# Kernel optimization log

Measured on AMD Instinct MI355X. Metric: run time of the kernel, lower is better.

The kernel has to match this reference:

```python
import jax, jax.numpy as jnp
import numpy as np

IN_SIZE, OUT_SIZE, EDGE_SIZE = 32, 32, 16
NET_LAYERS = [128, 128]          # cfg.net_layers (hidden sizes of the edge MLP)
B, N_NEIGH = 10000, 20           # nodes x neighbors
E = B * N_NEIGH                  # total edges


def setup_inputs() -> dict:
    key = jax.random.key(0)
    ks = jax.random.split(key, 16)
    h_v = jax.random.normal(ks[0], (B, N_NEIGH), jnp.float32)
    h_w = jax.random.normal(ks[1], (B, IN_SIZE), jnp.float32)
    e_vw = jax.random.normal(ks[2], (E, EDGE_SIZE), jnp.float32)
    dims = [EDGE_SIZE] + NET_LAYERS + [IN_SIZE * OUT_SIZE]
    params = {}
    for i, (din, dout) in enumerate(zip(dims[:-1], dims[1:])):
        bound = 1.0 / np.sqrt(din)  # torch nn.Linear default init
        params[f"W{i}"] = jax.random.uniform(ks[3 + 2 * i], (dout, din), jnp.float32, -bound, bound)
        params[f"b{i}"] = jax.random.uniform(ks[4 + 2 * i], (dout,), jnp.float32, -bound, bound)
    return {"h_v": h_v, "h_w": h_w, "e_vw": e_vw, **params}


def reference(h_v, h_w, e_vw, W0, b0, W1, b1, W2, b2):
    # Edge MLP: edge_size -> 128 -> 128 -> in*out (ReLU on hidden layers only)
    x = jax.nn.relu(e_vw @ W0.T + b0)
    x = jax.nn.relu(x @ W1.T + b1)
    m = (x @ W2.T + b2).reshape(-1, OUT_SIZE, IN_SIZE)  # [E, out, in]

    # Faithful reproduction of h_w[..., None].expand(B, in, n).view(-1, in)
    n = h_v.shape[1]
    h_w_rows = jnp.broadcast_to(h_w[:, :, None], (h_w.shape[0], IN_SIZE, n)).reshape(-1, IN_SIZE)  # [E, in]

    # bmm(m, h_w_rows[..., None]).squeeze() -> [E, out]
    out = jnp.einsum("eoi,ei->eo", m, h_w_rows)
    return jnp.squeeze(out)
```

## Files before the change

kernel.cpp:

```cpp
#include <hip/hip_runtime.h>


typedef __bf16 bf16x8 __attribute__((ext_vector_type(8)));
typedef float  f32x4  __attribute__((ext_vector_type(4)));

#define NB       10000
#define NNEIGH   20
#define PADH     136
#define NCHUNK   25

#define WS_W0S   0
#define WS_W1B   8192
#define WS_W2G   40960
#define WS_B2G   532480

__device__ __forceinline__ unsigned short f2bf(float f) {
    unsigned int u = __float_as_uint(f);
    unsigned int r = (u + 0x7fffu + ((u >> 16) & 1u)) >> 16;
    return (unsigned short)r;
}
__device__ __forceinline__ unsigned int pack2(float a, float b) {
    return (unsigned int)f2bf(a) | ((unsigned int)f2bf(b) << 16);
}

__global__ __launch_bounds__(256) void prep_kernel(
    const float* __restrict__ W0, const float* __restrict__ W1,
    const float* __restrict__ W2, const float* __restrict__ b2,
    unsigned short* __restrict__ w0s, unsigned short* __restrict__ w1b,
    unsigned short* __restrict__ w2g, float* __restrict__ b2g)
{
    const int bx = blockIdx.x, tid = threadIdx.x;
    if (bx < 960) {
        int gid = bx * 256 + tid;
        int kn = gid / 12288, rem = gid % 12288;
        int c = rem >> 7, k = rem & 127;
        int g = c >> 5, o = c & 31;
        int j0 = (32 * kn) / 20;
        int lo = 20 * (j0 + g) - 32 * kn;     if (lo < 0) lo = 0;
        int hi = 20 * (j0 + g + 1) - 32 * kn; if (hi > 32) hi = 32;
        float s = 0.f;
        for (int i = lo; i < hi; ++i) s += W2[(size_t)(32 * o + i) * 128 + k];
        w2g[gid] = f2bf(s);
    } else if (bx == 960) {
        for (int idx = tid; idx < 1920; idx += 256) {
            int kn = idx / 96, rem = idx - kn * 96;
            int g = rem >> 5, o = rem & 31;
            int j0 = (32 * kn) / 20;
            int lo = 20 * (j0 + g) - 32 * kn;     if (lo < 0) lo = 0;
            int hi = 20 * (j0 + g + 1) - 32 * kn; if (hi > 32) hi = 32;
            float s = 0.f;
            for (int i = lo; i < hi; ++i) s += b2[32 * o + i];
            b2g[idx] = s;
        }
    } else if (bx <= 962) {
        for (int i2 = tid; i2 < 2048; i2 += 256) {
            int idx = (bx - 961) * 2048 + i2;
            int ct = idx >> 9, lane = (idx >> 3) & 63, j = idx & 7;
            int lq = lane & 15, q = lane >> 4;
            int k = q * 8 + j;
            w0s[idx] = (k < 16) ? f2bf(W0[(ct * 16 + lq) * 16 + k]) : (unsigned short)0;
        }
    } else {
        int base = (bx - 963) * 1024;
        for (int i2 = tid; i2 < 1024; i2 += 256)
            w1b[base + i2] = f2bf(W1[base + i2]);
    }
}

__global__ __launch_bounds__(256, 2) void msg_kernel(
    const float* __restrict__ h_w, const float* __restrict__ e_vw,
    const float* __restrict__ b0v, const float* __restrict__ b1v,
    const unsigned short* __restrict__ w0s, const unsigned short* __restrict__ w1b,
    const unsigned short* __restrict__ w2g, const float* __restrict__ b2g,
    float* __restrict__ out)
{
    __shared__ __align__(16) unsigned short sW1[128 * PADH];
    __shared__ __align__(16) unsigned short sW2g[96 * PADH];
    __shared__ __align__(16) unsigned short sX[64 * PADH];

    const int tid = threadIdx.x;
    const int lane = tid & 63, w = tid >> 6;
    const int quad = lane >> 4, lq = lane & 15;
    const int kn = blockIdx.y, chunk = blockIdx.x;
    const int j0 = (32 * kn) / 20;

    {
        const uint4* src = (const uint4*)w1b;
        uint4* dst = (uint4*)sW1;
        for (int i = tid; i < 2048; i += 256) { int r = i >> 4, c = i & 15; dst[r * 17 + c] = src[i]; }
    }
    {
        const uint4* src = (const uint4*)(w2g + (size_t)kn * 96 * 128);
        uint4* dst = (uint4*)sW2g;
        for (int i = tid; i < 1536; i += 256) { int r = i >> 4, c = i & 15; dst[r * 17 + c] = src[i]; }
    }

    bf16x8 w0f[8];
#pragma unroll
    for (int ct = 0; ct < 8; ++ct)
        w0f[ct] = *(const bf16x8*)(w0s + (ct * 64 + lane) * 8);
    float b0r[8], b1r[8];
#pragma unroll
    for (int ct = 0; ct < 8; ++ct) {
        b0r[ct] = b0v[ct * 16 + lq];
        b1r[ct] = b1v[ct * 16 + lq];
    }
    float b2r[6];
#pragma unroll
    for (int i = 0; i < 6; ++i) {
        int g = i >> 1, half = i & 1;
        b2r[i] = b2g[kn * 96 + g * 32 + half * 16 + lq];
    }
    __syncthreads();

    const int rbase = w * 16;

    for (int btile = chunk; btile < 157; btile += NCHUNK) {
        const int bbase = btile * 64;
        const int rowE = bbase + rbase + lq;

        union { bf16x8 v; uint4 u; } A;
        A.u = make_uint4(0u, 0u, 0u, 0u);
        if (quad < 2 && rowE < NB) {
            const float4* p = (const float4*)(e_vw + ((size_t)rowE * NNEIGH + kn) * 16 + quad * 8);
            float4 f0 = p[0], f1 = p[1];
            A.u = make_uint4(pack2(f0.x, f0.y), pack2(f0.z, f0.w),
                             pack2(f1.x, f1.y), pack2(f1.z, f1.w));
        }

        float hwv[4][3];
#pragma unroll
        for (int r2 = 0; r2 < 4; ++r2) {
            int b = bbase + rbase + quad * 4 + r2;
#pragma unroll
            for (int g = 0; g < 3; ++g) {
                int jv = j0 + g; if (jv > 31) jv = 31;
                hwv[r2][g] = (b < NB) ? h_w[b * 32 + jv] : 0.f;
            }
        }

#pragma unroll
        for (int ct = 0; ct < 8; ++ct) {
            f32x4 acc = {0.f, 0.f, 0.f, 0.f};
            acc = __builtin_amdgcn_mfma_f32_16x16x32_bf16(A.v, w0f[ct], acc, 0, 0, 0);
#pragma unroll
            for (int r2 = 0; r2 < 4; ++r2) {
                float v = acc[r2] + b0r[ct];
                v = v > 0.f ? v : 0.f;
                sX[(rbase + quad * 4 + r2) * PADH + ct * 16 + lq] = f2bf(v);
            }
        }

        {
            bf16x8 af[4];
#pragma unroll
            for (int ka = 0; ka < 4; ++ka)
                af[ka] = *(const bf16x8*)&sX[(rbase + lq) * PADH + ka * 32 + quad * 8];
#pragma unroll
            for (int ct = 0; ct < 8; ++ct) {
                f32x4 acc = {0.f, 0.f, 0.f, 0.f};
#pragma unroll
                for (int ka = 0; ka < 4; ++ka) {
                    bf16x8 bf = *(const bf16x8*)&sW1[(ct * 16 + lq) * PADH + ka * 32 + quad * 8];
                    acc = __builtin_amdgcn_mfma_f32_16x16x32_bf16(af[ka], bf, acc, 0, 0, 0);
                }
#pragma unroll
                for (int r2 = 0; r2 < 4; ++r2) {
                    float v = acc[r2] + b1r[ct];
                    v = v > 0.f ? v : 0.f;
                    sX[(rbase + quad * 4 + r2) * PADH + ct * 16 + lq] = f2bf(v);
                }
            }
        }

        {
            bf16x8 af[4];
#pragma unroll
            for (int ka = 0; ka < 4; ++ka)
                af[ka] = *(const bf16x8*)&sX[(rbase + lq) * PADH + ka * 32 + quad * 8];
            f32x4 accC[6];
#pragma unroll
            for (int ct = 0; ct < 6; ++ct) {
                f32x4 acc = {0.f, 0.f, 0.f, 0.f};
#pragma unroll
                for (int ka = 0; ka < 4; ++ka) {
                    bf16x8 bf = *(const bf16x8*)&sW2g[(ct * 16 + lq) * PADH + ka * 32 + quad * 8];
                    acc = __builtin_amdgcn_mfma_f32_16x16x32_bf16(af[ka], bf, acc, 0, 0, 0);
                }
                accC[ct] = acc;
            }
#pragma unroll
            for (int half = 0; half < 2; ++half) {
#pragma unroll
                for (int r2 = 0; r2 < 4; ++r2) {
                    int b = bbase + rbase + quad * 4 + r2;
                    float oval = 0.f;
#pragma unroll
                    for (int g = 0; g < 3; ++g)
                        oval += hwv[r2][g] * (accC[g * 2 + half][r2] + b2r[g * 2 + half]);
                    if (b < NB)
                        out[((size_t)b * NNEIGH + kn) * 32 + half * 16 + lq] = oval;
                }
            }
        }
    }
}

extern "C" void kernel_launch(void* const* d_in, const int* in_sizes, int n_in,
                              void* d_out, int out_size, void* d_ws, size_t ws_size,
                              hipStream_t stream)
{
    const float* h_w = (const float*)d_in[1];
    const float* e_vw = (const float*)d_in[2];
    const float* W0 = (const float*)d_in[3];
    const float* b0 = (const float*)d_in[4];
    const float* W1 = (const float*)d_in[5];
    const float* b1 = (const float*)d_in[6];
    const float* W2 = (const float*)d_in[7];
    const float* b2 = (const float*)d_in[8];
    float* out = (float*)d_out;

    char* ws = (char*)d_ws;
    unsigned short* w0s = (unsigned short*)(ws + WS_W0S);
    unsigned short* w1b = (unsigned short*)(ws + WS_W1B);
    unsigned short* w2g = (unsigned short*)(ws + WS_W2G);
    float*          b2g = (float*)(ws + WS_B2G);

    prep_kernel<<<979, 256, 0, stream>>>(W0, W1, W2, b2, w0s, w1b, w2g, b2g);
    dim3 grid(NCHUNK, 20);
    msg_kernel<<<grid, 256, 0, stream>>>(h_w, e_vw, b0, b1, w0s, w1b, w2g, b2g, out);
}
```

Measured before the change: 134.2 us.

## Transpose MFMA operands, fold biases into accumulators, keep W2 in registers

New measurement: 183.7 us. +36.9%, slower.

```diff
diff --git a/kernel.cpp b/kernel.cpp
--- a/kernel.cpp
+++ b/kernel.cpp
@@ -6,7 +6,7 @@
 
 #define NB       10000
 #define NNEIGH   20
-#define PADH     136
+#define PADH     132
 #define NCHUNK   25
 
 #define WS_W0S   0
@@ -24,24 +24,48 @@
 }
 
 __global__ __launch_bounds__(256) void prep_kernel(
-    const float* __restrict__ W0, const float* __restrict__ W1,
+    const float* __restrict__ W0, const float* __restrict__ b0,
+    const float* __restrict__ W1,
     const float* __restrict__ W2, const float* __restrict__ b2,
     unsigned short* __restrict__ w0s, unsigned short* __restrict__ w1b,
     unsigned short* __restrict__ w2g, float* __restrict__ b2g)
 {
     const int bx = blockIdx.x, tid = threadIdx.x;
-    if (bx < 960) {
+    if (bx < 16) {
         int gid = bx * 256 + tid;
-        int kn = gid / 12288, rem = gid % 12288;
-        int c = rem >> 7, k = rem & 127;
-        int g = c >> 5, o = c & 31;
-        int j0 = (32 * kn) / 20;
-        int lo = 20 * (j0 + g) - 32 * kn;     if (lo < 0) lo = 0;
-        int hi = 20 * (j0 + g + 1) - 32 * kn; if (hi > 32) hi = 32;
-        float s = 0.f;
-        for (int i = lo; i < hi; ++i) s += W2[(size_t)(32 * o + i) * 128 + k];
-        w2g[gid] = f2bf(s);
-    } else if (bx == 960) {
+        int o = gid >> 7, k = gid & 127;
+        float pref[32];
+        float run = 0.f;
+#pragma unroll
+        for (int i = 0; i < 32; ++i) {
+            run += W2[(size_t)(32 * o + i) * 128 + k];
+            pref[i] = run;
+        }
+#pragma unroll
+        for (int kn = 0; kn < 20; ++kn) {
+            const int j0 = (32 * kn) / 20;
+#pragma unroll
+            for (int g = 0; g < 3; ++g) {
+                int lo = 20 * (j0 + g) - 32 * kn;     if (lo < 0) lo = 0;
+                int hi = 20 * (j0 + g + 1) - 32 * kn; if (hi > 32) hi = 32;
+                float v = (hi > lo) ? (pref[hi - 1] - (lo > 0 ? pref[lo - 1] : 0.f)) : 0.f;
+                w2g[((size_t)(kn * 3 + g) * 32 + o) * 128 + k] = f2bf(v);
+            }
+        }
+    } else if (bx == 16) {
+        for (int t = 0; t < 16; ++t) {
+            int idx = t * 256 + tid;
+            int ct = idx >> 9, lane = (idx >> 3) & 63, j = idx & 7;
+            int lq = lane & 15, q = lane >> 4;
+            int k = q * 8 + j, o = ct * 16 + lq;
+            float v = (k < 16) ? W0[o * 16 + k] : (k == 16 ? b0[o] : 0.f);
+            w0s[idx] = f2bf(v);
+        }
+    } else if (bx <= 32) {
+        int base = (bx - 17) * 1024;
+        for (int i2 = tid; i2 < 1024; i2 += 256)
+            w1b[base + i2] = f2bf(W1[base + i2]);
+    } else {
         for (int idx = tid; idx < 1920; idx += 256) {
             int kn = idx / 96, rem = idx - kn * 96;
             int g = rem >> 5, o = rem & 31;
@@ -52,30 +76,17 @@
             for (int i = lo; i < hi; ++i) s += b2[32 * o + i];
             b2g[idx] = s;
         }
-    } else if (bx <= 962) {
-        for (int i2 = tid; i2 < 2048; i2 += 256) {
-            int idx = (bx - 961) * 2048 + i2;
-            int ct = idx >> 9, lane = (idx >> 3) & 63, j = idx & 7;
-            int lq = lane & 15, q = lane >> 4;
-            int k = q * 8 + j;
-            w0s[idx] = (k < 16) ? f2bf(W0[(ct * 16 + lq) * 16 + k]) : (unsigned short)0;
-        }
-    } else {
-        int base = (bx - 963) * 1024;
-        for (int i2 = tid; i2 < 1024; i2 += 256)
-            w1b[base + i2] = f2bf(W1[base + i2]);
     }
 }
 
 __global__ __launch_bounds__(256, 2) void msg_kernel(
     const float* __restrict__ h_w, const float* __restrict__ e_vw,
-    const float* __restrict__ b0v, const float* __restrict__ b1v,
+    const float* __restrict__ b1v,
     const unsigned short* __restrict__ w0s, const unsigned short* __restrict__ w1b,
     const unsigned short* __restrict__ w2g, const float* __restrict__ b2g,
     float* __restrict__ out)
 {
     __shared__ __align__(16) unsigned short sW1[128 * PADH];
-    __shared__ __align__(16) unsigned short sW2g[96 * PADH];
     __shared__ __align__(16) unsigned short sX[64 * PADH];
 
     const int tid = threadIdx.x;
@@ -84,122 +95,121 @@
     const int kn = blockIdx.y, chunk = blockIdx.x;
     const int j0 = (32 * kn) / 20;
 
-    {
-        const uint4* src = (const uint4*)w1b;
-        uint4* dst = (uint4*)sW1;
-        for (int i = tid; i < 2048; i += 256) { int r = i >> 4, c = i & 15; dst[r * 17 + c] = src[i]; }
-    }
-    {
-        const uint4* src = (const uint4*)(w2g + (size_t)kn * 96 * 128);
-        uint4* dst = (uint4*)sW2g;
-        for (int i = tid; i < 1536; i += 256) { int r = i >> 4, c = i & 15; dst[r * 17 + c] = src[i]; }
-    }
-
+    bf16x8 w2gf[6][4];
+#pragma unroll
+    for (int ct = 0; ct < 6; ++ct)
+#pragma unroll
+        for (int ka = 0; ka < 4; ++ka)
+            w2gf[ct][ka] = *(const bf16x8*)(w2g + (size_t)(kn * 96 + ct * 16 + lq) * 128
+                                                 + ka * 32 + quad * 8);
     bf16x8 w0f[8];
 #pragma unroll
     for (int ct = 0; ct < 8; ++ct)
         w0f[ct] = *(const bf16x8*)(w0s + (ct * 64 + lane) * 8);
-    float b0r[8], b1r[8];
-#pragma unroll
-    for (int ct = 0; ct < 8; ++ct) {
-        b0r[ct] = b0v[ct * 16 + lq];
-        b1r[ct] = b1v[ct * 16 + lq];
-    }
-    float b2r[6];
-#pragma unroll
-    for (int i = 0; i < 6; ++i) {
-        int g = i >> 1, half = i & 1;
-        b2r[i] = b2g[kn * 96 + g * 32 + half * 16 + lq];
+    float4 b1r4[8];
+#pragma unroll
+    for (int ct = 0; ct < 8; ++ct)
+        b1r4[ct] = *(const float4*)(b1v + ct * 16 + quad * 4);
+    float4 b2r4[6];
+#pragma unroll
+    for (int ct = 0; ct < 6; ++ct)
+        b2r4[ct] = *(const float4*)(b2g + kn * 96 + ct * 16 + quad * 4);
+
+    {
+        const uint2* src = (const uint2*)w1b;
+        uint2* dst = (uint2*)sW1;
+        for (int i = tid; i < 4096; i += 256) {
+            int r = i >> 5, c = i & 31;
+            dst[r * 33 + c] = src[i];
+        }
     }
     __syncthreads();
 
     const int rbase = w * 16;
+    const unsigned short one_bf = 0x3f80;
 
     for (int btile = chunk; btile < 157; btile += NCHUNK) {
         const int bbase = btile * 64;
-        const int rowE = bbase + rbase + lq;
-
-        union { bf16x8 v; uint4 u; } A;
-        A.u = make_uint4(0u, 0u, 0u, 0u);
-        if (quad < 2 && rowE < NB) {
-            const float4* p = (const float4*)(e_vw + ((size_t)rowE * NNEIGH + kn) * 16 + quad * 8);
-            float4 f0 = p[0], f1 = p[1];
-            A.u = make_uint4(pack2(f0.x, f0.y), pack2(f0.z, f0.w),
-                             pack2(f1.x, f1.y), pack2(f1.z, f1.w));
-        }
-
-        float hwv[4][3];
-#pragma unroll
-        for (int r2 = 0; r2 < 4; ++r2) {
-            int b = bbase + rbase + quad * 4 + r2;
-#pragma unroll
-            for (int g = 0; g < 3; ++g) {
-                int jv = j0 + g; if (jv > 31) jv = 31;
-                hwv[r2][g] = (b < NB) ? h_w[b * 32 + jv] : 0.f;
-            }
+        const int e = bbase + rbase + lq;
+
+        union { bf16x8 v; uint4 u; } B;
+        B.u = make_uint4(0u, 0u, 0u, 0u);
+        if (quad < 2) {
+            if (e < NB) {
+                const float4* p = (const float4*)(e_vw + ((size_t)e * NNEIGH + kn) * 16 + quad * 8);
+                float4 f0 = p[0], f1 = p[1];
+                B.u = make_uint4(pack2(f0.x, f0.y), pack2(f0.z, f0.w),
+                                 pack2(f1.x, f1.y), pack2(f1.z, f1.w));
+            }
+        } else if (quad == 2) {
+            B.u.x = (unsigned int)one_bf;
+        }
+
+        float hwv[3];
+#pragma unroll
+        for (int g = 0; g < 3; ++g) {
+            int jv = j0 + g; if (jv > 31) jv = 31;
+            hwv[g] = (e < NB) ? h_w[(bbase + rbase + lq) * 32 + jv] : 0.f;
         }
 
 #pragma unroll
         for (int ct = 0; ct < 8; ++ct) {
             f32x4 acc = {0.f, 0.f, 0.f, 0.f};
-            acc = __builtin_amdgcn_mfma_f32_16x16x32_bf16(A.v, w0f[ct], acc, 0, 0, 0);
-#pragma unroll
-            for (int r2 = 0; r2 < 4; ++r2) {
-                float v = acc[r2] + b0r[ct];
-                v = v > 0.f ? v : 0.f;
-                sX[(rbase + quad * 4 + r2) * PADH + ct * 16 + lq] = f2bf(v);
-            }
+            acc = __builtin_amdgcn_mfma_f32_16x16x32_bf16(w0f[ct], B.v, acc, 0, 0, 0);
+#pragma unroll
+            for (int r2 = 0; r2 < 4; ++r2) acc[r2] = acc[r2] > 0.f ? acc[r2] : 0.f;
+            uint2 pk = make_uint2(pack2(acc[0], acc[1]), pack2(acc[2], acc[3]));
+            *(uint2*)&sX[(rbase + lq) * PADH + ct * 16 + quad * 4] = pk;
         }
 
         {
-            bf16x8 af[4];
+            bf16x8 xf[4];
 #pragma unroll
             for (int ka = 0; ka < 4; ++ka)
-                af[ka] = *(const bf16x8*)&sX[(rbase + lq) * PADH + ka * 32 + quad * 8];
+                xf[ka] = *(const bf16x8*)&sX[(rbase + lq) * PADH + ka * 32 + quad * 8];
 #pragma unroll
             for (int ct = 0; ct < 8; ++ct) {
-                f32x4 acc = {0.f, 0.f, 0.f, 0.f};
+                f32x4 acc = {b1r4[ct].x, b1r4[ct].y, b1r4[ct].z, b1r4[ct].w};
 #pragma unroll
                 for (int ka = 0; ka < 4; ++ka) {
-                    bf16x8 bf = *(const bf16x8*)&sW1[(ct * 16 + lq) * PADH + ka * 32 + quad * 8];
-                    acc = __builtin_amdgcn_mfma_f32_16x16x32_bf16(af[ka], bf, acc, 0, 0, 0);
+                    bf16x8 wf = *(const bf16x8*)&sW1[(ct * 16 + lq) * PADH + ka * 32 + quad * 8];
+                    acc = __builtin_amdgcn_mfma_f32_16x16x32_bf16(wf, xf[ka], acc, 0, 0, 0);
                 }
 #pragma unroll
-                for (int r2 = 0; r2 < 4; ++r2) {
-                    float v = acc[r2] + b1r[ct];
-                    v = v > 0.f ? v : 0.f;
-                    sX[(rbase + quad * 4 + r2) * PADH + ct * 16 + lq] = f2bf(v);
-                }
+                for (int r2 = 0; r2 < 4; ++r2) acc[r2] = acc[r2] > 0.f ? acc[r2] : 0.f;
+                uint2 pk = make_uint2(pack2(acc[0], acc[1]), pack2(acc[2], acc[3]));
+                *(uint2*)&sX[(rbase + lq) * PADH + ct * 16 + quad * 4] = pk;
             }
         }
 
         {
-            bf16x8 af[4];
+            bf16x8 xf[4];
 #pragma unroll
             for (int ka = 0; ka < 4; ++ka)
-                af[ka] = *(const bf16x8*)&sX[(rbase + lq) * PADH + ka * 32 + quad * 8];
+                xf[ka] = *(const bf16x8*)&sX[(rbase + lq) * PADH + ka * 32 + quad * 8];
             f32x4 accC[6];
 #pragma unroll
             for (int ct = 0; ct < 6; ++ct) {
-                f32x4 acc = {0.f, 0.f, 0.f, 0.f};
-#pragma unroll
-                for (int ka = 0; ka < 4; ++ka) {
-                    bf16x8 bf = *(const bf16x8*)&sW2g[(ct * 16 + lq) * PADH + ka * 32 + quad * 8];
-                    acc = __builtin_amdgcn_mfma_f32_16x16x32_bf16(af[ka], bf, acc, 0, 0, 0);
-                }
+                f32x4 acc = {b2r4[ct].x, b2r4[ct].y, b2r4[ct].z, b2r4[ct].w};
+#pragma unroll
+                for (int ka = 0; ka < 4; ++ka)
+                    acc = __builtin_amdgcn_mfma_f32_16x16x32_bf16(w2gf[ct][ka], xf[ka], acc, 0, 0, 0);
                 accC[ct] = acc;
             }
-#pragma unroll
-            for (int half = 0; half < 2; ++half) {
-#pragma unroll
-                for (int r2 = 0; r2 < 4; ++r2) {
-                    int b = bbase + rbase + quad * 4 + r2;
-                    float oval = 0.f;
-#pragma unroll
-                    for (int g = 0; g < 3; ++g)
-                        oval += hwv[r2][g] * (accC[g * 2 + half][r2] + b2r[g * 2 + half]);
-                    if (b < NB)
-                        out[((size_t)b * NNEIGH + kn) * 32 + half * 16 + lq] = oval;
+            if (e < NB) {
+#pragma unroll
+                for (int half = 0; half < 2; ++half) {
+                    float4 val;
+                    float* vp = &val.x;
+#pragma unroll
+                    for (int r2 = 0; r2 < 4; ++r2) {
+                        float s = 0.f;
+#pragma unroll
+                        for (int g = 0; g < 3; ++g)
+                            s += hwv[g] * accC[g * 2 + half][r2];
+                        vp[r2] = s;
+                    }
+                    *(float4*)(out + ((size_t)e * NNEIGH + kn) * 32 + half * 16 + quad * 4) = val;
                 }
             }
         }
@@ -226,7 +236,7 @@
     unsigned short* w2g = (unsigned short*)(ws + WS_W2G);
     float*          b2g = (float*)(ws + WS_B2G);
 
-    prep_kernel<<<979, 256, 0, stream>>>(W0, W1, W2, b2, w0s, w1b, w2g, b2g);
+    prep_kernel<<<34, 256, 0, stream>>>(W0, b0, W1, W2, b2, w0s, w1b, w2g, b2g);
     dim3 grid(NCHUNK, 20);
-    msg_kernel<<<grid, 256, 0, stream>>>(h_w, e_vw, b0, b1, w0s, w1b, w2g, b2g, out);
-}
+    msg_kernel<<<grid, 256, 0, stream>>>(h_w, e_vw, b1, w0s, w1b, w2g, b2g, out);
+}
```
